# Optimization experiments

Measured on AMD Instinct MI355X. Metric: run time of the kernel, lower is better.

The kernel has to match this reference:

```python
import jax, jax.numpy as jnp
import numpy as np

N, E, D, H, C, L = 50000, 600000, 128, 128, 64, 3
LN_EPS = 1e-5


def setup_inputs() -> dict:
    key = jax.random.key(0)
    ks = jax.random.split(key, 6)
    x = jax.random.normal(ks[0], (N, D), jnp.float32)
    edge_index = jax.random.randint(ks[1], (2, E), 0, N, jnp.int32)
    Wg = jax.random.normal(ks[2], (L, D, H), jnp.float32) * (1.0 / np.sqrt(D))
    bg = jnp.zeros((L, H), jnp.float32)
    ln_g = jnp.ones((L, H), jnp.float32)
    ln_b = jnp.zeros((L, H), jnp.float32)
    mlp_W1 = jax.random.normal(ks[3], (D + L * H, H), jnp.float32) * (1.0 / np.sqrt(D + L * H))
    mlp_b1 = jnp.zeros((H,), jnp.float32)
    mlp_W2 = jax.random.normal(ks[4], (H, C), jnp.float32) * (1.0 / np.sqrt(H))
    mlp_b2 = jnp.zeros((C,), jnp.float32)
    return {"x": x, "edge_index": edge_index, "Wg": Wg, "bg": bg,
            "ln_g": ln_g, "ln_b": ln_b, "mlp_W1": mlp_W1, "mlp_b1": mlp_b1,
            "mlp_W2": mlp_W2, "mlp_b2": mlp_b2}


def _layer_norm(h, g, b):
    mu = jnp.mean(h, axis=-1, keepdims=True)
    var = jnp.mean((h - mu) ** 2, axis=-1, keepdims=True)
    return g * (h - mu) * jax.lax.rsqrt(var + LN_EPS) + b


def _gcn(h, W, b, src, dst, dinv):
    # GCNConv with added self-loops and symmetric normalization:
    # out = D^{-1/2} (A + I) D^{-1/2} (h W) + b
    hW = h @ W                                   # [N, H]
    coef = (dinv[src] * dinv[dst])[:, None]      # [E, 1]
    agg = jax.ops.segment_sum(hW[src] * coef, dst, num_segments=N)
    agg = agg + hW * (dinv * dinv)[:, None]      # self-loop term
    return agg + b


def reference(x, edge_index, Wg, bg, ln_g, ln_b, mlp_W1, mlp_b1, mlp_W2, mlp_b2):
    src, dst = edge_index[0], edge_index[1]
    # degree including self-loop
    deg = jnp.ones((N,), x.dtype).at[dst].add(1.0)
    dinv = jax.lax.rsqrt(deg)
    feats = [x]
    h = x
    for i in range(L):  # small fixed layer count
        h = _gcn(h, Wg[i], bg[i], src, dst, dinv)
        h = _layer_norm(h, ln_g[i], ln_b[i])
        h = jax.nn.relu(h)
        feats.append(h)
    xc = jnp.concatenate(feats, axis=1)          # [N, D + L*H]
    z = jax.nn.relu(xc @ mlp_W1 + mlp_b1)
    z = z @ mlp_W2 + mlp_b2
    return jax.nn.softmax(z, axis=1)
```

## Files before the change

kernel.cpp:

```cpp
#include <hip/hip_runtime.h>
#include <math.h>

#define D 128
#define HH 128
#define CC 64
#define NLAYERS 3
#define LN_EPS 1e-5f

typedef __attribute__((ext_vector_type(8))) short bf16x8;
typedef __attribute__((ext_vector_type(4))) float f32x4;
typedef unsigned short u16;
typedef unsigned int u32;

__device__ __forceinline__ u16 f2bf(float f) {
    u32 u = __float_as_uint(f);
    u32 r = u + 0x7FFFu + ((u >> 16) & 1u);
    return (u16)(r >> 16);
}
__device__ __forceinline__ float bf2f(u16 h) {
    return __uint_as_float(((u32)h) << 16);
}

__device__ __forceinline__ void gload_lds16(const void* g, void* l) {
    __builtin_amdgcn_global_load_lds(
        (const __attribute__((address_space(1))) void*)g,
        (__attribute__((address_space(3))) void*)l, 16, 0, 0);
}

__global__ void k_prep(const float* __restrict__ x, u16* __restrict__ xh,
                       const float* __restrict__ Wg, u16* __restrict__ WgtH,
                       const float* __restrict__ W1, u16* __restrict__ W1tH,
                       const float* __restrict__ W2, u16* __restrict__ W2tH,
                       u16* __restrict__ W2tL,
                       const int* __restrict__ dst, int* __restrict__ cnt,
                       int N, int E)
{
    int i = blockIdx.x * blockDim.x + threadIdx.x;
    int nx4 = N * (D / 4);
    if (i < nx4) {
        float4 v = *(const float4*)(x + (size_t)i * 4);
        int row = i >> 5, c = (i & 31) << 2;
        ushort4 o;
        o.x = f2bf(v.x); o.y = f2bf(v.y); o.z = f2bf(v.z); o.w = f2bf(v.w);
        *(ushort4*)&xh[(size_t)row * 512 + c] = o;
        return;
    }
    i -= nx4;
    if (i < NLAYERS * D * HH) {
        int k = i >> 7, n = i & 127;
        int kc = k >> 5, q = (k >> 3) & 3, j = k & 7;
        WgtH[(((kc * 4 + q) << 7) + n) * 8 + j] = f2bf(Wg[i]);
        return;
    }
    i -= NLAYERS * D * HH;
    if (i < (D + NLAYERS * HH) * HH) {
        int k = i >> 7, n = i & 127;
        int kc = k >> 5, q = (k >> 3) & 3, j = k & 7;
        W1tH[(((kc * 4 + q) << 7) + n) * 8 + j] = f2bf(W1[i]);
        return;
    }
    i -= (D + NLAYERS * HH) * HH;
    if (i < HH * CC) {
        int k = i >> 6, n = i & 63;
        int kc = k >> 5, q = (k >> 3) & 3, j = k & 7;
        float v = W2[i];
        u16 h = f2bf(v);
        int o = (((kc * 4 + q) << 6) + n) * 8 + j;
        W2tH[o] = h;
        W2tL[o] = f2bf(v - bf2f(h));
        return;
    }
    i -= HH * CC;
    if (i < E) atomicAdd(&cnt[dst[i]], 1);
}


__global__ void k_scan_a(const int* __restrict__ cnt, int* __restrict__ rowptr,
                         int* __restrict__ bsum, int N) {
    __shared__ int ws[16];
    int tid  = threadIdx.x;
    int lane = tid & 63, wv = tid >> 6;
    int i = blockIdx.x * 1024 + tid;
    int v = (i < N) ? cnt[i] : 0;
    int incl = v;
    #pragma unroll
    for (int off = 1; off < 64; off <<= 1) {
        int u = __shfl_up(incl, off, 64);
        if (lane >= off) incl += u;
    }
    if (lane == 63) ws[wv] = incl;
    __syncthreads();
    if (wv == 0) {
        int s = (lane < 16) ? ws[lane] : 0;
        #pragma unroll
        for (int off = 1; off < 16; off <<= 1) {
            int u = __shfl_up(s, off, 64);
            if (lane >= off) s += u;
        }
        if (lane < 16) ws[lane] = s;
    }
    __syncthreads();
    int add = (wv == 0) ? 0 : ws[wv - 1];
    if (i < N) rowptr[i] = add + incl - v;
    if (tid == 1023) bsum[blockIdx.x] = ws[15];
}

__global__ void k_scan_c(int* __restrict__ rowptr, const int* __restrict__ bsum,
                         const int* __restrict__ cnt, float* __restrict__ dinv,
                         int* __restrict__ cursor, int N, int E, int nsb) {
    __shared__ int sb[64];
    if (threadIdx.x < 64) {
        int t = threadIdx.x;
        int v = (t < nsb) ? bsum[t] : 0;
        int incl = v;
        #pragma unroll
        for (int off = 1; off < 64; off <<= 1) {
            int u = __shfl_up(incl, off, 64);
            if (t >= off) incl += u;
        }
        sb[t] = incl - v;
    }
    __syncthreads();
    int i = blockIdx.x * blockDim.x + threadIdx.x;
    if (i < N) {
        int v = rowptr[i] + sb[i >> 10];
        rowptr[i] = v;
        cursor[i] = v;
        dinv[i] = rsqrtf(1.0f + (float)cnt[i]);
    }
    if (i == 0) rowptr[N] = E;
}

__global__ void k_scatter(const int* __restrict__ src, const int* __restrict__ dst,
                          const float* __restrict__ dinv,
                          int* __restrict__ cursor, int2* __restrict__ ecol, int E) {
    int i = blockIdx.x * blockDim.x + threadIdx.x;
    if (i < E) {
        int s = src[i], d = dst[i];
        int p = atomicAdd(&cursor[d], 1);
        float c = dinv[s] * dinv[d];
        ecol[p] = make_int2(s, __float_as_int(c));
    }
}

__global__ __launch_bounds__(256) void k_gemm_lf(
    const u16* __restrict__ A, int colOff,
    const u16* __restrict__ Bt, u16* __restrict__ OUTb, int N)
{
    __shared__ u16 sA[64 * 128];

    const int tid  = threadIdx.x;
    const int lane = tid & 63;
    const int wave = tid >> 6;
    const int wr   = wave & 1;
    const int wc   = wave >> 1;
    const int quad = lane >> 4;
    const int l15  = lane & 15;
    const int row0 = blockIdx.x * 64;

    #pragma unroll
    for (int rd = 0; rd < 4; ++rd) {
        int idx  = rd * 256 + tid;
        int row  = idx >> 4;
        int gp   = idx & 15;
        int gs   = gp ^ (row & 7);
        int grow = row0 + row; if (grow >= N) grow = N - 1;
        const u16* src = A + (size_t)grow * 512 + colOff + gs * 8;
        gload_lds16(src, &sA[(size_t)(rd * 256 + (tid & ~63)) * 8]);
    }

    const u16* pB = Bt + ((size_t)quad * 128 + wc * 64 + l15) * 8;
    bf16x8 bh[4][4];
    #pragma unroll
    for (int kc = 0; kc < 4; ++kc)
        #pragma unroll
        for (int j = 0; j < 4; ++j)
            bh[kc][j] = *(const bf16x8*)(pB + (size_t)kc * 4096 + j * 128);

    __syncthreads();

    const int rL[2] = { wr * 32 + l15, wr * 32 + 16 + l15 };
    bf16x8 ah[4][2];
    #pragma unroll
    for (int kc = 0; kc < 4; ++kc)
        #pragma unroll
        for (int i = 0; i < 2; ++i)
            ah[kc][i] = *(const bf16x8*)&sA[rL[i] * 128
                           + (((kc << 2) | quad) ^ (rL[i] & 7)) * 8];

    f32x4 acc[2][4];
    #pragma unroll
    for (int i = 0; i < 2; ++i)
        #pragma unroll
        for (int j = 0; j < 4; ++j)
            #pragma unroll
            for (int r = 0; r < 4; ++r) acc[i][j][r] = 0.f;

    #pragma unroll
    for (int kc = 0; kc < 4; ++kc)
        #pragma unroll
        for (int i = 0; i < 2; ++i)
            #pragma unroll
            for (int j = 0; j < 4; ++j)
                acc[i][j] = __builtin_amdgcn_mfma_f32_16x16x32_bf16(ah[kc][i], bh[kc][j], acc[i][j], 0, 0, 0);

    #pragma unroll
    for (int i = 0; i < 2; ++i)
        #pragma unroll
        for (int j = 0; j < 4; ++j) {
            int col = wc * 64 + j * 16 + l15;
            #pragma unroll
            for (int r = 0; r < 4; ++r) {
                int grow = row0 + wr * 32 + i * 16 + quad * 4 + r;
                if (grow < N)
                    OUTb[(size_t)grow * 128 + col] = f2bf(acc[i][j][r]);
            }
        }
}

__global__ __launch_bounds__(256) void k_mlp_fused(
    const u16* __restrict__ xcH,
    const u16* __restrict__ B1t, const float* __restrict__ b1,
    const u16* __restrict__ W2h, const u16* __restrict__ W2l,
    const float* __restrict__ b2, float* __restrict__ out, int N)
{
    __shared__ u16 sA[64 * 128];
    __shared__ u16 sZh[64 * 128];
    __shared__ u16 sZl[64 * 128];

    const int tid  = threadIdx.x;
    const int lane = tid & 63;
    const int wave = tid >> 6;
    const int wr   = wave & 1;
    const int wc   = wave >> 1;
    const int quad = lane >> 4;
    const int l15  = lane & 15;
    const int row0 = blockIdx.x * 64;

    const u16* pB = B1t + ((size_t)quad * 128 + wc * 64 + l15) * 8;
    const int rL[2] = { wr * 32 + l15, wr * 32 + 16 + l15 };

    f32x4 acc[2][4];
    #pragma unroll
    for (int i = 0; i < 2; ++i)
        #pragma unroll
        for (int j = 0; j < 4; ++j)
            #pragma unroll
            for (int r = 0; r < 4; ++r) acc[i][j][r] = 0.f;

    #pragma unroll
    for (int kp = 0; kp < 4; ++kp) {
        #pragma unroll
        for (int rd = 0; rd < 4; ++rd) {
            int idx  = rd * 256 + tid;
            int row  = idx >> 4;
            int gp   = idx & 15;
            int gs   = gp ^ (row & 7);
            int grow = row0 + row; if (grow >= N) grow = N - 1;
            const u16* src = xcH + (size_t)grow * 512 + kp * 128 + gs * 8;
            gload_lds16(src, &sA[(size_t)(rd * 256 + (tid & ~63)) * 8]);
        }
        bf16x8 bh[4][4];
        #pragma unroll
        for (int c = 0; c < 4; ++c)
            #pragma unroll
            for (int j = 0; j < 4; ++j)
                bh[c][j] = *(const bf16x8*)(pB + (size_t)(kp * 4 + c) * 4096 + j * 128);

        __syncthreads();

        bf16x8 ah[4][2];
        #pragma unroll
        for (int c = 0; c < 4; ++c)
            #pragma unroll
            for (int i = 0; i < 2; ++i)
                ah[c][i] = *(const bf16x8*)&sA[rL[i] * 128
                               + (((c << 2) | quad) ^ (rL[i] & 7)) * 8];

        #pragma unroll
        for (int c = 0; c < 4; ++c)
            #pragma unroll
            for (int i = 0; i < 2; ++i)
                #pragma unroll
                for (int j = 0; j < 4; ++j)
                    acc[i][j] = __builtin_amdgcn_mfma_f32_16x16x32_bf16(
                        ah[c][i], bh[c][j], acc[i][j], 0, 0, 0);

        __syncthreads();
    }

    #pragma unroll
    for (int jt = 0; jt < 4; ++jt) {
        int col = wc * 64 + jt * 16 + l15;
        float bv = b1[col];
        int qq = col >> 3, jj = col & 7;
        #pragma unroll
        for (int i = 0; i < 2; ++i) {
            #pragma unroll
            for (int rr = 0; rr < 4; ++rr) {
                int row = wr * 32 + i * 16 + quad * 4 + rr;
                float v = fmaxf(acc[i][jt][rr] + bv, 0.f);
                u16 h = f2bf(v);
                sZh[(qq * 64 + row) * 8 + jj] = h;
                sZl[(qq * 64 + row) * 8 + jj] = f2bf(v - bf2f(h));
            }
        }
    }
    __syncthreads();

    {
        f32x4 oacc[4];
        #pragma unroll
        for (int j = 0; j < 4; ++j)
            #pragma unroll
            for (int r = 0; r < 4; ++r) oacc[j][r] = 0.f;

        #pragma unroll
        for (int kc = 0; kc < 4; ++kc) {
            int qq = kc * 4 + quad;
            bf16x8 zh = *(const bf16x8*)&sZh[(qq * 64 + wave * 16 + l15) * 8];
            bf16x8 zl = *(const bf16x8*)&sZl[(qq * 64 + wave * 16 + l15) * 8];
            #pragma unroll
            for (int jt = 0; jt < 4; ++jt) {
                int n = jt * 16 + l15;
                bf16x8 wh = *(const bf16x8*)&W2h[(qq * 64 + n) * 8];
                bf16x8 wl = *(const bf16x8*)&W2l[(qq * 64 + n) * 8];
                oacc[jt] = __builtin_amdgcn_mfma_f32_16x16x32_bf16(zh, wh, oacc[jt], 0, 0, 0);
                oacc[jt] = __builtin_amdgcn_mfma_f32_16x16x32_bf16(zh, wl, oacc[jt], 0, 0, 0);
                oacc[jt] = __builtin_amdgcn_mfma_f32_16x16x32_bf16(zl, wh, oacc[jt], 0, 0, 0);
            }
        }

        #pragma unroll
        for (int jt = 0; jt < 4; ++jt) {
            float bv = b2[jt * 16 + l15];
            #pragma unroll
            for (int r = 0; r < 4; ++r) oacc[jt][r] += bv;
        }
        #pragma unroll
        for (int r = 0; r < 4; ++r) {
            float m = fmaxf(fmaxf(oacc[0][r], oacc[1][r]), fmaxf(oacc[2][r], oacc[3][r]));
            #pragma unroll
            for (int mask = 8; mask; mask >>= 1) m = fmaxf(m, __shfl_xor(m, mask, 64));
            float p0 = __expf(oacc[0][r] - m);
            float p1 = __expf(oacc[1][r] - m);
            float p2 = __expf(oacc[2][r] - m);
            float p3 = __expf(oacc[3][r] - m);
            float s = p0 + p1 + p2 + p3;
            #pragma unroll
            for (int mask = 8; mask; mask >>= 1) s += __shfl_xor(s, mask, 64);
            float inv = 1.0f / s;
            int grow = row0 + wave * 16 + quad * 4 + r;
            if (grow < N) {
                float* o = out + (size_t)grow * CC + l15;
                o[0]  = p0 * inv;
                o[16] = p1 * inv;
                o[32] = p2 * inv;
                o[48] = p3 * inv;
            }
        }
    }
}

__global__ __launch_bounds__(256, 8) void k_agg_ln(
    const u16* __restrict__ hWb,
    const int* __restrict__ rowptr, const int2* __restrict__ ecol,
    const float* __restrict__ dinv,
    const float* __restrict__ bg, const float* __restrict__ g,
    const float* __restrict__ b,
    u16* __restrict__ outHi, int N)
{
    const int lane = threadIdx.x & 63;
    const int c0   = (lane & 31) << 2;

    const float4 bgv = *(const float4*)(bg + c0);
    const float4 gv  = *(const float4*)(g + c0);
    const float4 bv  = *(const float4*)(b + c0);

    const int nslots = gridDim.x * 8;
    for (int wid = blockIdx.x * 8 + ((threadIdx.x >> 6) << 1) + (lane >> 5);
         wid < N; wid += nslots) {
        float di = dinv[wid];
        float sc = di * di;

        uint2 hv = *(const uint2*)(hWb + (size_t)wid * HH + c0);
        float a0 = bf2f((u16)hv.x) * sc;
        float a1 = bf2f((u16)(hv.x >> 16)) * sc;
        float a2 = bf2f((u16)hv.y) * sc;
        float a3 = bf2f((u16)(hv.y >> 16)) * sc;
        float q0 = 0.f, q1 = 0.f, q2 = 0.f, q3 = 0.f;

        int e0 = rowptr[wid];
        int m  = rowptr[wid + 1] - e0;
        const int2* ep = ecol + e0;

        int k = 0;
        for (; k + 4 <= m; k += 4) {
            int2 p[4];
            uint2 v[4];
            #pragma unroll
            for (int t = 0; t < 4; ++t) p[t] = ep[k + t];
            #pragma unroll
            for (int t = 0; t < 4; ++t)
                v[t] = *(const uint2*)(hWb + (size_t)p[t].x * HH + c0);
            #pragma unroll
            for (int t = 0; t < 4; ++t) {
                float c = __int_as_float(p[t].y);
                float x0 = bf2f((u16)v[t].x) * c;
                float x1 = bf2f((u16)(v[t].x >> 16)) * c;
                float x2 = bf2f((u16)v[t].y) * c;
                float x3 = bf2f((u16)(v[t].y >> 16)) * c;
                if (t & 1) { q0 += x0; q1 += x1; q2 += x2; q3 += x3; }
                else       { a0 += x0; a1 += x1; a2 += x2; a3 += x3; }
            }
        }
        if (k < m) {
            int2 p0 = ep[k];
            int2 p1 = (k + 1 < m) ? ep[k + 1] : p0;
            int2 p2 = (k + 2 < m) ? ep[k + 2] : p0;
            uint2 v0 = *(const uint2*)(hWb + (size_t)p0.x * HH + c0);
            uint2 v1 = *(const uint2*)(hWb + (size_t)p1.x * HH + c0);
            uint2 v2 = *(const uint2*)(hWb + (size_t)p2.x * HH + c0);
            float cc0 = __int_as_float(p0.y);
            float cc1 = (k + 1 < m) ? __int_as_float(p1.y) : 0.f;
            float cc2 = (k + 2 < m) ? __int_as_float(p2.y) : 0.f;
            a0 += bf2f((u16)v0.x) * cc0;  a1 += bf2f((u16)(v0.x >> 16)) * cc0;
            a2 += bf2f((u16)v0.y) * cc0;  a3 += bf2f((u16)(v0.y >> 16)) * cc0;
            q0 += bf2f((u16)v1.x) * cc1;  q1 += bf2f((u16)(v1.x >> 16)) * cc1;
            q2 += bf2f((u16)v1.y) * cc1;  q3 += bf2f((u16)(v1.y >> 16)) * cc1;
            a0 += bf2f((u16)v2.x) * cc2;  a1 += bf2f((u16)(v2.x >> 16)) * cc2;
            a2 += bf2f((u16)v2.y) * cc2;  a3 += bf2f((u16)(v2.y >> 16)) * cc2;
        }
        a0 += q0; a1 += q1; a2 += q2; a3 += q3;
        a0 += bgv.x; a1 += bgv.y; a2 += bgv.z; a3 += bgv.w;

        float ssum = (a0 + a1) + (a2 + a3);
        #pragma unroll
        for (int off = 16; off; off >>= 1) ssum += __shfl_xor(ssum, off, 64);
        float mu = ssum * (1.0f / 128.0f);
        float d0 = a0 - mu, d1 = a1 - mu, d2 = a2 - mu, d3 = a3 - mu;
        float vsum = (d0 * d0 + d1 * d1) + (d2 * d2 + d3 * d3);
        #pragma unroll
        for (int off = 16; off; off >>= 1) vsum += __shfl_xor(vsum, off, 64);
        float rstd = rsqrtf(vsum * (1.0f / 128.0f) + LN_EPS);

        float o0 = fmaxf(gv.x * d0 * rstd + bv.x, 0.f);
        float o1 = fmaxf(gv.y * d1 * rstd + bv.y, 0.f);
        float o2 = fmaxf(gv.z * d2 * rstd + bv.z, 0.f);
        float o3 = fmaxf(gv.w * d3 * rstd + bv.w, 0.f);
        uint2 o;
        o.x = (u32)f2bf(o0) | ((u32)f2bf(o1) << 16);
        o.y = (u32)f2bf(o2) | ((u32)f2bf(o3) << 16);
        *(uint2*)&outHi[(size_t)wid * 512 + c0] = o;
    }
}

extern "C" void kernel_launch(void* const* d_in, const int* in_sizes, int n_in,
                              void* d_out, int out_size, void* d_ws, size_t ws_size,
                              hipStream_t stream) {
    const float* x   = (const float*)d_in[0];
    const int*   ei  = (const int*)  d_in[1];
    const float* Wg  = (const float*)d_in[2];
    const float* bg  = (const float*)d_in[3];
    const float* lng = (const float*)d_in[4];
    const float* lnb = (const float*)d_in[5];
    const float* W1  = (const float*)d_in[6];
    const float* b1  = (const float*)d_in[7];
    const float* W2  = (const float*)d_in[8];
    const float* b2  = (const float*)d_in[9];
    float* out = (float*)d_out;

    const int N = in_sizes[0] / D;
    const int E = in_sizes[1] / 2;
    const int* srcp = ei;
    const int* dstp = ei + E;

    char* ws = (char*)d_ws;
    size_t off = 0;
    auto alloc = [&](size_t bytes) -> void* {
        void* p = ws + off;
        off += (bytes + 511) & ~(size_t)511;
        return p;
    };
    int*   cnt    = (int*)  alloc((size_t)N * 4);
    int*   rowptr = (int*)  alloc((size_t)(N + 1) * 4);
    int*   cursor = (int*)  alloc((size_t)N * 4);
    int*   bsum   = (int*)  alloc(64 * 4);
    int2*  ecol   = (int2*) alloc((size_t)E * 8);
    float* dinv   = (float*)alloc((size_t)N * 4);
    u16*   hWb    = (u16*)  alloc((size_t)N * HH * 2);
    u16*   xcH    = (u16*)  alloc((size_t)N * 512 * 2);
    u16*   WgtH   = (u16*)  alloc((size_t)NLAYERS * D * HH * 2);
    u16*   W1tH   = (u16*)  alloc((size_t)(D + NLAYERS * HH) * HH * 2);
    u16*   W2tH   = (u16*)  alloc((size_t)HH * CC * 2);
    u16*   W2tL   = (u16*)  alloc((size_t)HH * CC * 2);

    const int B = 256;
    const int gE = (E + B - 1) / B;
    const int nsb = (N + 1023) / 1024;

    hipMemsetAsync(cnt, 0, (size_t)N * 4, stream);

    const int prepTotal = N * (D / 4) + NLAYERS * D * HH
                        + (D + NLAYERS * HH) * HH + HH * CC + E;
    k_prep<<<(prepTotal + B - 1) / B, B, 0, stream>>>(x, xcH, Wg, WgtH, W1, W1tH,
                                                      W2, W2tH, W2tL, dstp, cnt, N, E);
    k_scan_a<<<nsb, 1024, 0, stream>>>(cnt, rowptr, bsum, N);
    k_scan_c<<<(N + B - 1) / B, B, 0, stream>>>(rowptr, bsum, cnt, dinv, cursor, N, E, nsb);
    k_scatter<<<gE, B, 0, stream>>>(srcp, dstp, dinv, cursor, ecol, E);

    const int gemmBlocks = (N + 63) / 64;
    const int mlpBlocks  = (N + 63) / 64;
    const int aggBlocks  = 2048;

    for (int l = 0; l < NLAYERS; ++l) {
        k_gemm_lf<<<gemmBlocks, B, 0, stream>>>(xcH, l * HH,
                                                WgtH + (size_t)l * D * HH, hWb, N);
        k_agg_ln<<<aggBlocks, B, 0, stream>>>(hWb, rowptr, ecol, dinv,
                                              bg + (size_t)l * HH,
                                              lng + (size_t)l * HH,
                                              lnb + (size_t)l * HH,
                                              xcH + (size_t)(l + 1) * HH, N);
    }

    k_mlp_fused<<<mlpBlocks, B, 0, stream>>>(xcH, W1tH, b1,
                                             W2tH, W2tL, b2, out, N);
}
```

Measured before the change: 294.0 us.

## Double-buffer LDS tiles in layer GEMM and MLP kernels to overlap loads

The layer GEMM now handles 128 rows per block. It prefetches the second 64-row A tile into a second LDS buffer while the first tile is computed, which halves the grid and amortizes the weight register loads. The fused MLP kernel double-buffers its four K panels, so the next panel's global-to-LDS load is issued before the current panel's MFMAs, and it drops one barrier per iteration. It also reuses the two staging buffers for the bf16 hi/lo Z tiles, cutting LDS use from 48KB to 32KB, which may allow more blocks per CU. Correctness depends on the barrier waiting for the async LDS loads, and the larger GEMM blocks reduce the number of blocks available for load balancing.

```diff
diff --git a/kernel.cpp b/kernel.cpp
--- a/kernel.cpp
+++ b/kernel.cpp
@@ -147,7 +147,96 @@
     const u16* __restrict__ A, int colOff,
     const u16* __restrict__ Bt, u16* __restrict__ OUTb, int N)
 {
-    __shared__ u16 sA[64 * 128];
+    __shared__ u16 sA[2][64 * 128];
+
+    const int tid  = threadIdx.x;
+    const int lane = tid & 63;
+    const int wave = tid >> 6;
+    const int wr   = wave & 1;
+    const int wc   = wave >> 1;
+    const int quad = lane >> 4;
+    const int l15  = lane & 15;
+    const int row0 = blockIdx.x * 128;
+
+    #define STAGE_A(buf, base)                                                  \
+        {                                                                       \
+            _Pragma("unroll")                                                   \
+            for (int rd = 0; rd < 4; ++rd) {                                    \
+                int idx  = rd * 256 + tid;                                      \
+                int row  = idx >> 4;                                            \
+                int gp   = idx & 15;                                            \
+                int gs   = gp ^ (row & 7);                                      \
+                int grow = (base) + row; if (grow >= N) grow = N - 1;           \
+                const u16* srcp_ = A + (size_t)grow * 512 + colOff + gs * 8;    \
+                gload_lds16(srcp_, &sA[buf][(size_t)(rd * 256 + (tid & ~63)) * 8]); \
+            }                                                                   \
+        }
+
+    STAGE_A(0, row0)
+
+    const u16* pB = Bt + ((size_t)quad * 128 + wc * 64 + l15) * 8;
+    bf16x8 bh[4][4];
+    #pragma unroll
+    for (int kc = 0; kc < 4; ++kc)
+        #pragma unroll
+        for (int j = 0; j < 4; ++j)
+            bh[kc][j] = *(const bf16x8*)(pB + (size_t)kc * 4096 + j * 128);
+
+    const int rL[2] = { wr * 32 + l15, wr * 32 + 16 + l15 };
+
+    #pragma unroll
+    for (int t = 0; t < 2; ++t) {
+        __syncthreads();
+        if (t == 0) STAGE_A(1, row0 + 64)
+
+        bf16x8 ah[4][2];
+        #pragma unroll
+        for (int kc = 0; kc < 4; ++kc)
+            #pragma unroll
+            for (int i = 0; i < 2; ++i)
+                ah[kc][i] = *(const bf16x8*)&sA[t][rL[i] * 128
+                               + (((kc << 2) | quad) ^ (rL[i] & 7)) * 8];
+
+        f32x4 acc[2][4];
+        #pragma unroll
+        for (int i = 0; i < 2; ++i)
+            #pragma unroll
+            for (int j = 0; j < 4; ++j)
+                #pragma unroll
+                for (int r = 0; r < 4; ++r) acc[i][j][r] = 0.f;
+
+        #pragma unroll
+        for (int kc = 0; kc < 4; ++kc)
+            #pragma unroll
+            for (int i = 0; i < 2; ++i)
+                #pragma unroll
+                for (int j = 0; j < 4; ++j)
+                    acc[i][j] = __builtin_amdgcn_mfma_f32_16x16x32_bf16(
+                        ah[kc][i], bh[kc][j], acc[i][j], 0, 0, 0);
+
+        #pragma unroll
+        for (int i = 0; i < 2; ++i)
+            #pragma unroll
+            for (int j = 0; j < 4; ++j) {
+                int col = wc * 64 + j * 16 + l15;
+                #pragma unroll
+                for (int r = 0; r < 4; ++r) {
+                    int grow = row0 + t * 64 + wr * 32 + i * 16 + quad * 4 + r;
+                    if (grow < N)
+                        OUTb[(size_t)grow * 128 + col] = f2bf(acc[i][j][r]);
+                }
+            }
+    }
+    #undef STAGE_A
+}
+
+__global__ __launch_bounds__(256) void k_mlp_fused(
+    const u16* __restrict__ xcH,
+    const u16* __restrict__ B1t, const float* __restrict__ b1,
+    const u16* __restrict__ W2h, const u16* __restrict__ W2l,
+    const float* __restrict__ b2, float* __restrict__ out, int N)
+{
+    __shared__ u16 smem[2][64 * 128];
 
     const int tid  = threadIdx.x;
     const int lane = tid & 63;
@@ -158,35 +247,22 @@
     const int l15  = lane & 15;
     const int row0 = blockIdx.x * 64;
 
-    #pragma unroll
-    for (int rd = 0; rd < 4; ++rd) {
-        int idx  = rd * 256 + tid;
-        int row  = idx >> 4;
-        int gp   = idx & 15;
-        int gs   = gp ^ (row & 7);
-        int grow = row0 + row; if (grow >= N) grow = N - 1;
-        const u16* src = A + (size_t)grow * 512 + colOff + gs * 8;
-        gload_lds16(src, &sA[(size_t)(rd * 256 + (tid & ~63)) * 8]);
-    }
-
-    const u16* pB = Bt + ((size_t)quad * 128 + wc * 64 + l15) * 8;
-    bf16x8 bh[4][4];
-    #pragma unroll
-    for (int kc = 0; kc < 4; ++kc)
-        #pragma unroll
-        for (int j = 0; j < 4; ++j)
-            bh[kc][j] = *(const bf16x8*)(pB + (size_t)kc * 4096 + j * 128);
-
-    __syncthreads();
-
+    #define STAGE_K(buf, kp)                                                    \
+        {                                                                       \
+            _Pragma("unroll")                                                   \
+            for (int rd = 0; rd < 4; ++rd) {                                    \
+                int idx  = rd * 256 + tid;                                      \
+                int row  = idx >> 4;                                            \
+                int gp   = idx & 15;                                            \
+                int gs   = gp ^ (row & 7);                                      \
+                int grow = row0 + row; if (grow >= N) grow = N - 1;             \
+                const u16* srcp_ = xcH + (size_t)grow * 512 + (kp) * 128 + gs * 8; \
+                gload_lds16(srcp_, &smem[buf][(size_t)(rd * 256 + (tid & ~63)) * 8]); \
+            }                                                                   \
+        }
+
+    const u16* pB = B1t + ((size_t)quad * 128 + wc * 64 + l15) * 8;
     const int rL[2] = { wr * 32 + l15, wr * 32 + 16 + l15 };
-    bf16x8 ah[4][2];
-    #pragma unroll
-    for (int kc = 0; kc < 4; ++kc)
-        #pragma unroll
-        for (int i = 0; i < 2; ++i)
-            ah[kc][i] = *(const bf16x8*)&sA[rL[i] * 128
-                           + (((kc << 2) | quad) ^ (rL[i] & 7)) * 8];
 
     f32x4 acc[2][4];
     #pragma unroll
@@ -196,70 +272,13 @@
             #pragma unroll
             for (int r = 0; r < 4; ++r) acc[i][j][r] = 0.f;
 
-    #pragma unroll
-    for (int kc = 0; kc < 4; ++kc)
-        #pragma unroll
-        for (int i = 0; i < 2; ++i)
-            #pragma unroll
-            for (int j = 0; j < 4; ++j)
-                acc[i][j] = __builtin_amdgcn_mfma_f32_16x16x32_bf16(ah[kc][i], bh[kc][j], acc[i][j], 0, 0, 0);
-
-    #pragma unroll
-    for (int i = 0; i < 2; ++i)
-        #pragma unroll
-        for (int j = 0; j < 4; ++j) {
-            int col = wc * 64 + j * 16 + l15;
-            #pragma unroll
-            for (int r = 0; r < 4; ++r) {
-                int grow = row0 + wr * 32 + i * 16 + quad * 4 + r;
-                if (grow < N)
-                    OUTb[(size_t)grow * 128 + col] = f2bf(acc[i][j][r]);
-            }
-        }
-}
-
-__global__ __launch_bounds__(256) void k_mlp_fused(
-    const u16* __restrict__ xcH,
-    const u16* __restrict__ B1t, const float* __restrict__ b1,
-    const u16* __restrict__ W2h, const u16* __restrict__ W2l,
-    const float* __restrict__ b2, float* __restrict__ out, int N)
-{
-    __shared__ u16 sA[64 * 128];
-    __shared__ u16 sZh[64 * 128];
-    __shared__ u16 sZl[64 * 128];
-
-    const int tid  = threadIdx.x;
-    const int lane = tid & 63;
-    const int wave = tid >> 6;
-    const int wr   = wave & 1;
-    const int wc   = wave >> 1;
-    const int quad = lane >> 4;
-    const int l15  = lane & 15;
-    const int row0 = blockIdx.x * 64;
-
-    const u16* pB = B1t + ((size_t)quad * 128 + wc * 64 + l15) * 8;
-    const int rL[2] = { wr * 32 + l15, wr * 32 + 16 + l15 };
-
-    f32x4 acc[2][4];
-    #pragma unroll
-    for (int i = 0; i < 2; ++i)
-        #pragma unroll
-        for (int j = 0; j < 4; ++j)
-            #pragma unroll
-            for (int r = 0; r < 4; ++r) acc[i][j][r] = 0.f;
+    STAGE_K(0, 0)
 
     #pragma unroll
     for (int kp = 0; kp < 4; ++kp) {
-        #pragma unroll
-        for (int rd = 0; rd < 4; ++rd) {
-            int idx  = rd * 256 + tid;
-            int row  = idx >> 4;
-            int gp   = idx & 15;
-            int gs   = gp ^ (row & 7);
-            int grow = row0 + row; if (grow >= N) grow = N - 1;
-            const u16* src = xcH + (size_t)grow * 512 + kp * 128 + gs * 8;
-            gload_lds16(src, &sA[(size_t)(rd * 256 + (tid & ~63)) * 8]);
-        }
+        __syncthreads();
+        if (kp < 3) STAGE_K((kp + 1) & 1, kp + 1)
+
         bf16x8 bh[4][4];
         #pragma unroll
         for (int c = 0; c < 4; ++c)
@@ -267,14 +286,12 @@
             for (int j = 0; j < 4; ++j)
                 bh[c][j] = *(const bf16x8*)(pB + (size_t)(kp * 4 + c) * 4096 + j * 128);
 
-        __syncthreads();
-
         bf16x8 ah[4][2];
         #pragma unroll
         for (int c = 0; c < 4; ++c)
             #pragma unroll
             for (int i = 0; i < 2; ++i)
-                ah[c][i] = *(const bf16x8*)&sA[rL[i] * 128
+                ah[c][i] = *(const bf16x8*)&smem[kp & 1][rL[i] * 128
                                + (((c << 2) | quad) ^ (rL[i] & 7)) * 8];
 
         #pragma unroll
@@ -285,9 +302,12 @@
                 for (int j = 0; j < 4; ++j)
                     acc[i][j] = __builtin_amdgcn_mfma_f32_16x16x32_bf16(
                         ah[c][i], bh[c][j], acc[i][j], 0, 0, 0);
-
-        __syncthreads();
-    }
+    }
+    #undef STAGE_K
+
+    __syncthreads();
+    u16* sZh = smem[0];
+    u16* sZl = smem[1];
 
     #pragma unroll
     for (int jt = 0; jt < 4; ++jt) {
@@ -509,7 +529,7 @@
     k_scan_c<<<(N + B - 1) / B, B, 0, stream>>>(rowptr, bsum, cnt, dinv, cursor, N, E, nsb);
     k_scatter<<<gE, B, 0, stream>>>(srcp, dstp, dinv, cursor, ecol, E);
 
-    const int gemmBlocks = (N + 63) / 64;
+    const int gemmBlocks = (N + 127) / 128;
     const int mlpBlocks  = (N + 63) / 64;
     const int aggBlocks  = 2048;
 
```

Measured after the change: 289.2 us (median of 2 runs). No clear change (-1.6%).
